# Performance work log

Hardware: AMD Instinct MI355X
Metric: run time of the kernel (lower is better)

Reference implementation:

```python
import jax, jax.numpy as jnp
import numpy as np

NE = 200000   # num_entities
NR = 16       # num_relations
D  = 128      # embed_dim
B  = 4096     # batch
S  = 64       # neighbors per node
L  = 2        # num_layers
H  = 4        # attention heads (hardcoded in module)


def _ln(x, g, b, eps=1e-5):
    m = jnp.mean(x, -1, keepdims=True)
    v = jnp.mean((x - m) ** 2, -1, keepdims=True)
    return (x - m) * jax.lax.rsqrt(v + eps) * g + b


def setup_inputs() -> dict:
    key = jax.random.key(0)
    ks = jax.random.split(key, 12)
    s = 0.05
    return {
        'drug_entity_indices': jax.random.randint(ks[0], (B,), 0, NE),
        'adj_entity': jax.random.randint(ks[1], (B, S), 0, NE),
        'adj_relation': jax.random.randint(ks[2], (B, S), 0, NR),
        'edge_weights': jax.random.uniform(ks[3], (B, S), dtype=jnp.float32),
        'entity_emb': jax.random.normal(ks[4], (NE, D), jnp.float32) * s,
        'W_rgcn': jax.random.normal(ks[5], (L, NR, D, D), jnp.float32) * s,
        'res_w': jax.random.normal(ks[6], (L, D, D), jnp.float32) * s,
        'res_b': jnp.zeros((L, D), jnp.float32),
        'proj_w': jax.random.normal(ks[7], (L, D, D), jnp.float32) * s,
        'proj_b': jnp.zeros((L, D), jnp.float32),
        'ln_g': jnp.ones((L, D), jnp.float32),
        'ln_b': jnp.zeros((L, D), jnp.float32),
        'in_proj_w': jax.random.normal(ks[8], (3 * D, D), jnp.float32) * s,
        'in_proj_b': jnp.zeros((3 * D,), jnp.float32),
        'out_proj_w': jax.random.normal(ks[9], (D, D), jnp.float32) * s,
        'out_proj_b': jnp.zeros((D,), jnp.float32),
        'fln_g': jnp.ones((D,), jnp.float32),
        'fln_b': jnp.zeros((D,), jnp.float32),
    }


def reference(drug_entity_indices, adj_entity, adj_relation, edge_weights,
              entity_emb, W_rgcn, res_w, res_b, proj_w, proj_b, ln_g, ln_b,
              in_proj_w, in_proj_b, out_proj_w, out_proj_b, fln_g, fln_b):
    node = entity_emb[drug_entity_indices]           # [B,D] combined_emb
    nbr = entity_emb[adj_entity]                     # [B,S,D]
    # Route each edge to its relation: sum_s nbr*ew*[rel==r] then one GEMM per relation
    # (mathematically identical to the per-relation masked matmul loop in torch).
    onehot = jax.nn.one_hot(adj_relation, NR, dtype=node.dtype)      # [B,S,R]
    pre = jnp.einsum('bsd,bsr->brd', nbr * edge_weights[..., None], onehot)
    outs = []
    for l in range(L):
        msgs = jnp.einsum('brd,rde->be', pre, W_rgcn[l])             # [B,D]
        h = jax.nn.relu(node + msgs + node @ res_w[l].T + res_b[l])  # RGCNAggregator
        node = _ln(h @ proj_w[l].T + proj_b[l] + node, ln_g[l], ln_b[l])
        outs.append(node)
    x = jnp.stack(outs, 0)                           # [L,B,D] seq-first
    qkv = x @ in_proj_w.T + in_proj_b
    q, k, v = jnp.split(qkv, 3, axis=-1)
    hd = D // H
    def heads(t):
        return t.reshape(L, B, H, hd).transpose(1, 2, 0, 3)          # [B,H,L,hd]
    q, k, v = heads(q), heads(k), heads(v)
    att = jax.nn.softmax(jnp.einsum('bhld,bhmd->bhlm', q, k) / np.sqrt(hd).astype(np.float32), axis=-1)
    o = jnp.einsum('bhlm,bhmd->bhld', att, v).transpose(2, 0, 1, 3).reshape(L, B, D)
    o = o @ out_proj_w.T + out_proj_b
    return _ln(o.mean(0), fln_g, fln_b)              # [B,D]
```

## Files before the change

kernel.cpp:

```cpp
#include <hip/hip_runtime.h>
#include <math.h>

#define NRREL 16
#define DDIM 128
#define BBATCH 4096
#define SNBR 64
#define ROWS 8

typedef __attribute__((ext_vector_type(8))) short short8;
typedef __attribute__((ext_vector_type(4))) float floatx4;

__device__ __forceinline__ unsigned short f2bf(float f) {
    unsigned u = __builtin_bit_cast(unsigned, f);
    u += 0x7fffu + ((u >> 16) & 1u);
    return (unsigned short)(u >> 16);
}
__device__ __forceinline__ float bf2f(unsigned short u) {
    return __builtin_bit_cast(float, ((unsigned)u) << 16);
}

extern "C" __global__ __launch_bounds__(256)
void k_prep(const float* __restrict__ W_rgcn,
            const float* __restrict__ res_w, const float* __restrict__ proj_w,
            const float* __restrict__ in_w, const float* __restrict__ out_w,
            unsigned short* __restrict__ Wcat, unsigned short* __restrict__ resw,
            unsigned short* __restrict__ projw, unsigned short* __restrict__ inw,
            unsigned short* __restrict__ outw)
{
    __shared__ float tileT[64 * 65];
    const int bid = blockIdx.x, t = threadIdx.x;

    if (bid < 128) {
        const int l = bid >> 6, rem = bid & 63;
        const int k0 = (rem >> 1) * 64, e0 = (rem & 1) * 64;
        #pragma unroll
        for (int i = 0; i < 4; ++i) {
            int flat = t + 256 * i;
            int k = flat >> 4, c = flat & 15;
            float4 v = *(const float4*)(W_rgcn + ((size_t)(l * 2048 + k0 + k)) * 128 + e0 + 4 * c);
            tileT[(4 * c + 0) * 65 + k] = v.x;
            tileT[(4 * c + 1) * 65 + k] = v.y;
            tileT[(4 * c + 2) * 65 + k] = v.z;
            tileT[(4 * c + 3) * 65 + k] = v.w;
        }
        __syncthreads();
        const int e = t >> 2, m = t & 3;
        #pragma unroll
        for (int half = 0; half < 2; ++half) {
            int kk = 16 * m + 8 * half;
            short8 o;
            #pragma unroll
            for (int j = 0; j < 8; ++j) o[j] = (short)f2bf(tileT[e * 65 + kk + j]);
            *(short8*)(Wcat + ((size_t)(l * 128 + e0 + e)) * 2048 + k0 + kk) = o;
        }
    } else {
        int j4 = ((bid - 128) * 256 + t) * 4;
        const float* src; unsigned short* dst; int off;
        if (j4 < 32768)       { src = res_w;  dst = resw;  off = j4; }
        else if (j4 < 65536)  { src = proj_w; dst = projw; off = j4 - 32768; }
        else if (j4 < 114688) { src = in_w;   dst = inw;   off = j4 - 65536; }
        else                  { src = out_w;  dst = outw;  off = j4 - 114688; }
        float4 v = *(const float4*)(src + off);
        ushort4 o = { f2bf(v.x), f2bf(v.y), f2bf(v.z), f2bf(v.w) };
        *(ushort4*)(dst + off) = o;
    }
}

extern "C" __global__ __launch_bounds__(512)
void k_fused(const int* __restrict__ drug, const int* __restrict__ adj_e,
             const int* __restrict__ adj_r, const float* __restrict__ ew,
             const float* __restrict__ emb,
             const unsigned short* __restrict__ Wcat,
             const unsigned short* __restrict__ resw, const unsigned short* __restrict__ projw,
             const float* __restrict__ res_b, const float* __restrict__ proj_b,
             const float* __restrict__ ln_g, const float* __restrict__ ln_b,
             const unsigned short* __restrict__ inw, const float* __restrict__ in_b,
             const unsigned short* __restrict__ outw, const float* __restrict__ out_b,
             const float* __restrict__ fg, const float* __restrict__ fb,
             float* __restrict__ outp)
{
    __shared__ union {
        struct { unsigned short preA[ROWS * 2056]; } a;
        struct {
            unsigned short h_b16[ROWS * 136];
            unsigned short xs_l[2 * ROWS * 136];
            unsigned short qkvl[2 * ROWS * 392];
        } t;
    } sm;
    __shared__ float node_ln[ROWS * 132];
    __shared__ unsigned short node_b16[ROWS * 136];
    __shared__ union {
        struct {
            int   cnt[ROWS][16];
            int   strt[ROWS][16];
            int   sperm[ROWS][64];
            float wperm[ROWS][64];
        } g;
        float msum[ROWS * 260];
    } sg;
    __shared__ float psum[8][8], psq[8][8];

    const int t = threadIdx.x, w = t >> 6, lane = t & 63, l15 = lane & 15, q = lane >> 4;
    const int r0 = blockIdx.x * ROWS;

    const int erow = t >> 6, es = t & 63;
    int   ent0 = adj_e[(r0 + erow) * SNBR + es];
    float ewt0 = ew[(r0 + erow) * SNBR + es];
    int   rel0 = adj_r[(r0 + erow) * SNBR + es];
    if (t < 128) sg.g.cnt[t >> 4][t & 15] = 0;
    if (t < 256) {
        int rr = t >> 5, c = t & 31;
        int di = drug[r0 + rr];
        float4 v = *(const float4*)(emb + (size_t)di * DDIM + 4 * c);
        *(float4*)(node_ln + rr * 132 + 4 * c) = v;
        ushort4 o = { f2bf(v.x), f2bf(v.y), f2bf(v.z), f2bf(v.w) };
        *(ushort4*)(node_b16 + rr * 136 + 4 * c) = o;
    }
    __syncthreads();

    atomicAdd(&sg.g.cnt[erow][rel0], 1);
    __syncthreads();

    if (t < ROWS) {
        int a = 0;
        #pragma unroll
        for (int r = 0; r < NRREL; ++r) { sg.g.strt[t][r] = a; a += sg.g.cnt[t][r]; }
    }
    __syncthreads();

    {
        int pos0 = atomicAdd(&sg.g.strt[erow][rel0], 1);
        sg.g.sperm[erow][pos0] = ent0;
        sg.g.wperm[erow][pos0] = ewt0;
    }
    __syncthreads();

    {
        #pragma unroll 1
        for (int i = 0; i < 4; ++i) {
            int u = t + 512 * i;
            int row = u >> 8, rl = (u >> 4) & 15, g8 = u & 15;
            int n = sg.g.cnt[row][rl];
            int end = sg.g.strt[row][rl];
            int beg = end - n;
            float acc[8] = {0.f, 0.f, 0.f, 0.f, 0.f, 0.f, 0.f, 0.f};
            #pragma unroll 1
            for (int jb = beg; jb < end; jb += 8) {
                const float* pp[8]; float wq[8];
                #pragma unroll
                for (int u2 = 0; u2 < 8; ++u2) {
                    int live = (jb + u2 < end);
                    int j = live ? jb + u2 : beg;
                    wq[u2] = live ? sg.g.wperm[row][j] : 0.f;
                    pp[u2] = emb + (size_t)sg.g.sperm[row][j] * DDIM + 8 * g8;
                }
                float4 v0[8], v1[8];
                #pragma unroll
                for (int u2 = 0; u2 < 8; ++u2) {
                    v0[u2] = *(const float4*)pp[u2];
                    v1[u2] = *(const float4*)(pp[u2] + 4);
                }
                #pragma unroll
                for (int u2 = 0; u2 < 8; ++u2) {
                    acc[0] = fmaf(v0[u2].x, wq[u2], acc[0]); acc[1] = fmaf(v0[u2].y, wq[u2], acc[1]);
                    acc[2] = fmaf(v0[u2].z, wq[u2], acc[2]); acc[3] = fmaf(v0[u2].w, wq[u2], acc[3]);
                    acc[4] = fmaf(v1[u2].x, wq[u2], acc[4]); acc[5] = fmaf(v1[u2].y, wq[u2], acc[5]);
                    acc[6] = fmaf(v1[u2].z, wq[u2], acc[6]); acc[7] = fmaf(v1[u2].w, wq[u2], acc[7]);
                }
            }
            short8 o;
            #pragma unroll
            for (int jj = 0; jj < 8; ++jj) o[jj] = (short)f2bf(acc[jj]);
            *(short8*)(sm.a.preA + row * 2056 + rl * DDIM + 8 * g8) = o;
        }
    }
    __syncthreads();

    {
        floatx4 macc[2] = {};
        const unsigned short* ap = sm.a.preA + (l15 & 7) * 2056 + 8 * q;
        const unsigned short* bp = Wcat + (size_t)(32 * w + l15) * 2048 + 8 * q;
        #pragma unroll 8
        for (int k = 0; k < 2048; k += 32) {
            short8 A = *(const short8*)(ap + k);
            #pragma unroll
            for (int ni = 0; ni < 2; ++ni) {
                short8 B = *(const short8*)(bp + (size_t)(ni * 16) * 2048 + k);
                macc[ni] = __builtin_amdgcn_mfma_f32_16x16x32_bf16(A, B, macc[ni], 0, 0, 0);
            }
        }
        if (q < 2) {
            #pragma unroll
            for (int ni = 0; ni < 2; ++ni) {
                int gc = 32 * w + ni * 16 + l15;
                #pragma unroll
                for (int r = 0; r < 4; ++r)
                    sg.msum[(4 * q + r) * 260 + gc] = macc[ni][r];
            }
        }
    }
    __syncthreads();

    for (int l = 0; l < 2; ++l) {
        {
            const unsigned short* Bw = resw + (size_t)l * DDIM * DDIM;
            floatx4 acc = {};
            const unsigned short* ap = node_b16 + (l15 & 7) * 136 + 8 * q;
            #pragma unroll
            for (int kk = 0; kk < DDIM; kk += 32) {
                short8 A = *(const short8*)(ap + kk);
                short8 B = *(const short8*)(Bw + (size_t)(16 * w + l15) * DDIM + kk + 8 * q);
                acc = __builtin_amdgcn_mfma_f32_16x16x32_bf16(A, B, acc, 0, 0, 0);
            }
            int gc = 16 * w + l15;
            float rb = res_b[l * DDIM + gc];
            if (q < 2) {
                #pragma unroll
                for (int r = 0; r < 4; ++r) {
                    int lr = 4 * q + r;
                    float v = acc[r] + rb + node_ln[lr * 132 + gc] + sg.msum[lr * 260 + l * DDIM + gc];
                    sm.t.h_b16[lr * 136 + gc] = f2bf(v > 0.f ? v : 0.f);
                }
            }
        }
        __syncthreads();
        {
            const unsigned short* Bw = projw + (size_t)l * DDIM * DDIM;
            floatx4 acc = {};
            const unsigned short* ap = sm.t.h_b16 + (l15 & 7) * 136 + 8 * q;
            #pragma unroll
            for (int kk = 0; kk < DDIM; kk += 32) {
                short8 A = *(const short8*)(ap + kk);
                short8 B = *(const short8*)(Bw + (size_t)(16 * w + l15) * DDIM + kk + 8 * q);
                acc = __builtin_amdgcn_mfma_f32_16x16x32_bf16(A, B, acc, 0, 0, 0);
            }
            int gc = 16 * w + l15;
            float vv[4];
            float s4[4] = {0, 0, 0, 0}, sq4[4] = {0, 0, 0, 0};
            float pb = proj_b[l * DDIM + gc];
            if (q < 2) {
                #pragma unroll
                for (int r = 0; r < 4; ++r) {
                    float v = acc[r] + pb + node_ln[(4 * q + r) * 132 + gc];
                    vv[r] = v; s4[r] = v; sq4[r] = v * v;
                }
            }
            #pragma unroll
            for (int r = 0; r < 4; ++r)
                #pragma unroll
                for (int off2 = 8; off2 >= 1; off2 >>= 1) {
                    s4[r] += __shfl_xor(s4[r], off2, 64);
                    sq4[r] += __shfl_xor(sq4[r], off2, 64);
                }
            if (l15 == 0 && q < 2) {
                #pragma unroll
                for (int r = 0; r < 4; ++r) {
                    psum[w][4 * q + r] = s4[r];
                    psq[w][4 * q + r] = sq4[r];
                }
            }
            __syncthreads();
            float g2 = ln_g[l * DDIM + gc], bb = ln_b[l * DDIM + gc];
            if (q < 2) {
                #pragma unroll
                for (int r = 0; r < 4; ++r) {
                    int lr = 4 * q + r;
                    float ssum = 0.f, ssq = 0.f;
                    #pragma unroll
                    for (int ww = 0; ww < 8; ++ww) { ssum += psum[ww][lr]; ssq += psq[ww][lr]; }
                    float mean = ssum * (1.f / DDIM);
                    float var = ssq * (1.f / DDIM) - mean * mean;
                    float val = (vv[r] - mean) * rsqrtf(var + 1e-5f) * g2 + bb;
                    node_ln[lr * 132 + gc] = val;
                    unsigned short ub = f2bf(val);
                    node_b16[lr * 136 + gc] = ub;
                    sm.t.xs_l[(2 * lr + l) * 136 + gc] = ub;
                }
            }
            __syncthreads();
        }
    }

    {
        floatx4 acc[3] = {};
        const unsigned short* ap = sm.t.xs_l + l15 * 136 + 8 * q;
        #pragma unroll
        for (int kk = 0; kk < DDIM; kk += 32) {
            short8 A = *(const short8*)(ap + kk);
            #pragma unroll
            for (int ni = 0; ni < 3; ++ni) {
                short8 B = *(const short8*)(inw + (size_t)(48 * w + ni * 16 + l15) * DDIM + kk + 8 * q);
                acc[ni] = __builtin_amdgcn_mfma_f32_16x16x32_bf16(A, B, acc[ni], 0, 0, 0);
            }
        }
        #pragma unroll
        for (int ni = 0; ni < 3; ++ni) {
            int gc = 48 * w + ni * 16 + l15;
            float ib = in_b[gc];
            #pragma unroll
            for (int r = 0; r < 4; ++r)
                sm.t.qkvl[(4 * q + r) * 392 + gc] = f2bf(acc[ni][r] + ib);
        }
    }
    __syncthreads();

    if (t < 64) {
        int g4 = t >> 3, j = t & 7;
        const unsigned short* row0 = sm.t.qkvl + (2 * g4) * 392;
        const unsigned short* row1 = row0 + 392;
        float p00 = 0.f, p01 = 0.f, p10 = 0.f, p11 = 0.f;
        #pragma unroll
        for (int dd = 0; dd < 16; ++dd) {
            int d = 16 * j + dd;
            float q0 = bf2f(row0[d]), k0 = bf2f(row0[128 + d]);
            float q1 = bf2f(row1[d]), k1 = bf2f(row1[128 + d]);
            p00 = fmaf(q0, k0, p00); p01 = fmaf(q0, k1, p01);
            p10 = fmaf(q1, k0, p10); p11 = fmaf(q1, k1, p11);
        }
        p00 += __shfl_xor(p00, 1, 64); p01 += __shfl_xor(p01, 1, 64);
        p10 += __shfl_xor(p10, 1, 64); p11 += __shfl_xor(p11, 1, 64);
        const float sc = 0.17677669529663687f;
        p00 *= sc; p01 *= sc; p10 *= sc; p11 *= sc;
        float m0 = fmaxf(p00, p01), e00 = expf(p00 - m0), e01 = expf(p01 - m0);
        float i0 = 1.f / (e00 + e01);
        float m1 = fmaxf(p10, p11), e10 = expf(p10 - m1), e11 = expf(p11 - m1);
        float i1 = 1.f / (e10 + e11);
        #pragma unroll
        for (int dd = 0; dd < 16; ++dd) {
            int d = 16 * j + dd;
            float v0 = bf2f(row0[256 + d]), v1 = bf2f(row1[256 + d]);
            sm.t.xs_l[(2 * g4) * 136 + d]     = f2bf((e00 * v0 + e01 * v1) * i0);
            sm.t.xs_l[(2 * g4 + 1) * 136 + d] = f2bf((e10 * v0 + e11 * v1) * i1);
        }
    }
    __syncthreads();

    {
        floatx4 acc = {};
        const unsigned short* ap = sm.t.xs_l + l15 * 136 + 8 * q;
        #pragma unroll
        for (int kk = 0; kk < DDIM; kk += 32) {
            short8 A = *(const short8*)(ap + kk);
            short8 B = *(const short8*)(outw + (size_t)(16 * w + l15) * DDIM + kk + 8 * q);
            acc = __builtin_amdgcn_mfma_f32_16x16x32_bf16(A, B, acc, 0, 0, 0);
        }
        int gc = 16 * w + l15;
        float ob = out_b[gc];
        float av[2];
        float s2[2], sq2[2];
        #pragma unroll
        for (int rr = 0; rr < 2; ++rr) {
            float v = 0.5f * (acc[2 * rr] + acc[2 * rr + 1]) + ob;
            av[rr] = v; s2[rr] = v; sq2[rr] = v * v;
        }
        #pragma unroll
        for (int rr = 0; rr < 2; ++rr)
            #pragma unroll
            for (int off2 = 8; off2 >= 1; off2 >>= 1) {
                s2[rr] += __shfl_xor(s2[rr], off2, 64);
                sq2[rr] += __shfl_xor(sq2[rr], off2, 64);
            }
        if (l15 == 0) {
            #pragma unroll
            for (int rr = 0; rr < 2; ++rr) {
                psum[w][2 * q + rr] = s2[rr];
                psq[w][2 * q + rr] = sq2[rr];
            }
        }
        __syncthreads();
        float g2 = fg[gc], bb = fb[gc];
        #pragma unroll
        for (int rr = 0; rr < 2; ++rr) {
            int idx = 2 * q + rr;
            float ssum = 0.f, ssq = 0.f;
            #pragma unroll
            for (int ww = 0; ww < 8; ++ww) { ssum += psum[ww][idx]; ssq += psq[ww][idx]; }
            float mean = ssum * (1.f / DDIM);
            float var = ssq * (1.f / DDIM) - mean * mean;
            outp[(size_t)(r0 + idx) * DDIM + gc] = (av[rr] - mean) * rsqrtf(var + 1e-5f) * g2 + bb;
        }
    }
}

extern "C" void kernel_launch(void* const* d_in, const int* in_sizes, int n_in,
                              void* d_out, int out_size, void* d_ws, size_t ws_size,
                              hipStream_t stream) {
    const int*   drug_idx = (const int*)d_in[0];
    const int*   adj_ent  = (const int*)d_in[1];
    const int*   adj_rel  = (const int*)d_in[2];
    const float* ew       = (const float*)d_in[3];
    const float* emb      = (const float*)d_in[4];
    const float* W_rgcn   = (const float*)d_in[5];
    const float* res_w    = (const float*)d_in[6];
    const float* res_b    = (const float*)d_in[7];
    const float* proj_w   = (const float*)d_in[8];
    const float* proj_b   = (const float*)d_in[9];
    const float* ln_g     = (const float*)d_in[10];
    const float* ln_b     = (const float*)d_in[11];
    const float* in_w     = (const float*)d_in[12];
    const float* in_b     = (const float*)d_in[13];
    const float* out_w    = (const float*)d_in[14];
    const float* out_b    = (const float*)d_in[15];
    const float* fg       = (const float*)d_in[16];
    const float* fb       = (const float*)d_in[17];
    float* outp = (float*)d_out;

    char* ws = (char*)d_ws;
    size_t off = 0;
    auto alloc = [&](size_t bytes) { size_t o = off; off = (off + bytes + 255) & ~(size_t)255; return o; };
    unsigned short* Wcat    = (unsigned short*)(ws + alloc((size_t)256 * 2048 * 2));
    unsigned short* resw    = (unsigned short*)(ws + alloc((size_t)2 * 128 * 128 * 2));
    unsigned short* projw   = (unsigned short*)(ws + alloc((size_t)2 * 128 * 128 * 2));
    unsigned short* inw     = (unsigned short*)(ws + alloc((size_t)384 * 128 * 2));
    unsigned short* outw    = (unsigned short*)(ws + alloc((size_t)128 * 128 * 2));

    hipLaunchKernelGGL(k_prep, dim3(256), dim3(256), 0, stream,
                       W_rgcn, res_w, proj_w, in_w, out_w,
                       Wcat, resw, projw, inw, outw);
    hipLaunchKernelGGL(k_fused, dim3(BBATCH / ROWS), dim3(512), 0, stream,
                       drug_idx, adj_ent, adj_rel, ew, emb,
                       Wcat, resw, projw, res_b, proj_b, ln_g, ln_b,
                       inw, in_b, outw, out_b, fg, fb, outp);
}
```

Measured before the change: 261.9 us.

## Process 16 batch rows per block with 1024 threads to fill MFMA tiles

Doubles the rows handled per block from 8 to 16 and the block size from 512 to 1024 threads. The 16x16 MFMA row dimension is now fully used instead of half wasted, so each Wcat weight tile streamed from global memory serves twice as many rows. The per-layer GEMMs, QKV projection, output projection and layer-norm reductions are remapped across 16 waves, with some waves idle in the smaller stages. Shared memory per block roughly doubles and the grid halves, which can lower occupancy and the number of blocks available to spread across CUs.

```diff
diff --git a/kernel.cpp b/kernel.cpp
--- a/kernel.cpp
+++ b/kernel.cpp
@@ -5,7 +5,7 @@
 #define DDIM 128
 #define BBATCH 4096
 #define SNBR 64
-#define ROWS 8
+#define ROWS 16
 
 typedef __attribute__((ext_vector_type(8))) short short8;
 typedef __attribute__((ext_vector_type(4))) float floatx4;
@@ -66,7 +66,7 @@
     }
 }
 
-extern "C" __global__ __launch_bounds__(512)
+extern "C" __global__ __launch_bounds__(1024)
 void k_fused(const int* __restrict__ drug, const int* __restrict__ adj_e,
              const int* __restrict__ adj_r, const float* __restrict__ ew,
              const float* __restrict__ emb,
@@ -98,7 +98,7 @@
         } g;
         float msum[ROWS * 260];
     } sg;
-    __shared__ float psum[8][8], psq[8][8];
+    __shared__ float psum[16][16], psq[16][16];
 
     const int t = threadIdx.x, w = t >> 6, lane = t & 63, l15 = lane & 15, q = lane >> 4;
     const int r0 = blockIdx.x * ROWS;
@@ -107,8 +107,8 @@
     int   ent0 = adj_e[(r0 + erow) * SNBR + es];
     float ewt0 = ew[(r0 + erow) * SNBR + es];
     int   rel0 = adj_r[(r0 + erow) * SNBR + es];
-    if (t < 128) sg.g.cnt[t >> 4][t & 15] = 0;
-    if (t < 256) {
+    if (t < 256) sg.g.cnt[t >> 4][t & 15] = 0;
+    if (t < 512) {
         int rr = t >> 5, c = t & 31;
         int di = drug[r0 + rr];
         float4 v = *(const float4*)(emb + (size_t)di * DDIM + 4 * c);
@@ -138,7 +138,7 @@
     {
         #pragma unroll 1
         for (int i = 0; i < 4; ++i) {
-            int u = t + 512 * i;
+            int u = t + 1024 * i;
             int row = u >> 8, rl = (u >> 4) & 15, g8 = u & 15;
             int n = sg.g.cnt[row][rl];
             int end = sg.g.strt[row][rl];
@@ -177,35 +177,27 @@
     __syncthreads();
 
     {
-        floatx4 macc[2] = {};
-        const unsigned short* ap = sm.a.preA + (l15 & 7) * 2056 + 8 * q;
-        const unsigned short* bp = Wcat + (size_t)(32 * w + l15) * 2048 + 8 * q;
+        floatx4 macc = {};
+        const unsigned short* ap = sm.a.preA + l15 * 2056 + 8 * q;
+        const unsigned short* bp = Wcat + (size_t)(16 * w + l15) * 2048 + 8 * q;
         #pragma unroll 8
         for (int k = 0; k < 2048; k += 32) {
             short8 A = *(const short8*)(ap + k);
-            #pragma unroll
-            for (int ni = 0; ni < 2; ++ni) {
-                short8 B = *(const short8*)(bp + (size_t)(ni * 16) * 2048 + k);
-                macc[ni] = __builtin_amdgcn_mfma_f32_16x16x32_bf16(A, B, macc[ni], 0, 0, 0);
-            }
-        }
-        if (q < 2) {
-            #pragma unroll
-            for (int ni = 0; ni < 2; ++ni) {
-                int gc = 32 * w + ni * 16 + l15;
-                #pragma unroll
-                for (int r = 0; r < 4; ++r)
-                    sg.msum[(4 * q + r) * 260 + gc] = macc[ni][r];
-            }
-        }
+            short8 B = *(const short8*)(bp + k);
+            macc = __builtin_amdgcn_mfma_f32_16x16x32_bf16(A, B, macc, 0, 0, 0);
+        }
+        int gc = 16 * w + l15;
+        #pragma unroll
+        for (int r = 0; r < 4; ++r)
+            sg.msum[(4 * q + r) * 260 + gc] = macc[r];
     }
     __syncthreads();
 
     for (int l = 0; l < 2; ++l) {
-        {
+        if (w < 8) {
             const unsigned short* Bw = resw + (size_t)l * DDIM * DDIM;
             floatx4 acc = {};
-            const unsigned short* ap = node_b16 + (l15 & 7) * 136 + 8 * q;
+            const unsigned short* ap = node_b16 + l15 * 136 + 8 * q;
             #pragma unroll
             for (int kk = 0; kk < DDIM; kk += 32) {
                 short8 A = *(const short8*)(ap + kk);
@@ -214,54 +206,52 @@
             }
             int gc = 16 * w + l15;
             float rb = res_b[l * DDIM + gc];
-            if (q < 2) {
-                #pragma unroll
-                for (int r = 0; r < 4; ++r) {
-                    int lr = 4 * q + r;
-                    float v = acc[r] + rb + node_ln[lr * 132 + gc] + sg.msum[lr * 260 + l * DDIM + gc];
-                    sm.t.h_b16[lr * 136 + gc] = f2bf(v > 0.f ? v : 0.f);
-                }
+            #pragma unroll
+            for (int r = 0; r < 4; ++r) {
+                int lr = 4 * q + r;
+                float v = acc[r] + rb + node_ln[lr * 132 + gc] + sg.msum[lr * 260 + l * DDIM + gc];
+                sm.t.h_b16[lr * 136 + gc] = f2bf(v > 0.f ? v : 0.f);
             }
         }
         __syncthreads();
         {
-            const unsigned short* Bw = projw + (size_t)l * DDIM * DDIM;
-            floatx4 acc = {};
-            const unsigned short* ap = sm.t.h_b16 + (l15 & 7) * 136 + 8 * q;
-            #pragma unroll
-            for (int kk = 0; kk < DDIM; kk += 32) {
-                short8 A = *(const short8*)(ap + kk);
-                short8 B = *(const short8*)(Bw + (size_t)(16 * w + l15) * DDIM + kk + 8 * q);
-                acc = __builtin_amdgcn_mfma_f32_16x16x32_bf16(A, B, acc, 0, 0, 0);
-            }
+            float vv[4];
             int gc = 16 * w + l15;
-            float vv[4];
-            float s4[4] = {0, 0, 0, 0}, sq4[4] = {0, 0, 0, 0};
-            float pb = proj_b[l * DDIM + gc];
-            if (q < 2) {
+            if (w < 8) {
+                const unsigned short* Bw = projw + (size_t)l * DDIM * DDIM;
+                floatx4 acc = {};
+                const unsigned short* ap = sm.t.h_b16 + l15 * 136 + 8 * q;
+                #pragma unroll
+                for (int kk = 0; kk < DDIM; kk += 32) {
+                    short8 A = *(const short8*)(ap + kk);
+                    short8 B = *(const short8*)(Bw + (size_t)(16 * w + l15) * DDIM + kk + 8 * q);
+                    acc = __builtin_amdgcn_mfma_f32_16x16x32_bf16(A, B, acc, 0, 0, 0);
+                }
+                float s4[4], sq4[4];
+                float pb = proj_b[l * DDIM + gc];
                 #pragma unroll
                 for (int r = 0; r < 4; ++r) {
                     float v = acc[r] + pb + node_ln[(4 * q + r) * 132 + gc];
                     vv[r] = v; s4[r] = v; sq4[r] = v * v;
                 }
-            }
-            #pragma unroll
-            for (int r = 0; r < 4; ++r)
-                #pragma unroll
-                for (int off2 = 8; off2 >= 1; off2 >>= 1) {
-                    s4[r] += __shfl_xor(s4[r], off2, 64);
-                    sq4[r] += __shfl_xor(sq4[r], off2, 64);
-                }
-            if (l15 == 0 && q < 2) {
-                #pragma unroll
-                for (int r = 0; r < 4; ++r) {
-                    psum[w][4 * q + r] = s4[r];
-                    psq[w][4 * q + r] = sq4[r];
+                #pragma unroll
+                for (int r = 0; r < 4; ++r)
+                    #pragma unroll
+                    for (int off2 = 8; off2 >= 1; off2 >>= 1) {
+                        s4[r] += __shfl_xor(s4[r], off2, 64);
+                        sq4[r] += __shfl_xor(sq4[r], off2, 64);
+                    }
+                if (l15 == 0) {
+                    #pragma unroll
+                    for (int r = 0; r < 4; ++r) {
+                        psum[w][4 * q + r] = s4[r];
+                        psq[w][4 * q + r] = sq4[r];
+                    }
                 }
             }
             __syncthreads();
-            float g2 = ln_g[l * DDIM + gc], bb = ln_b[l * DDIM + gc];
-            if (q < 2) {
+            if (w < 8) {
+                float g2 = ln_g[l * DDIM + gc], bb = ln_b[l * DDIM + gc];
                 #pragma unroll
                 for (int r = 0; r < 4; ++r) {
                     int lr = 4 * q + r;
@@ -281,30 +271,30 @@
         }
     }
 
-    {
-        floatx4 acc[3] = {};
-        const unsigned short* ap = sm.t.xs_l + l15 * 136 + 8 * q;
+    if (w < 12) {
+        floatx4 acc[4] = {};
+        const unsigned short* ap = sm.t.xs_l + (16 * (w & 1) + l15) * 136 + 8 * q;
         #pragma unroll
         for (int kk = 0; kk < DDIM; kk += 32) {
             short8 A = *(const short8*)(ap + kk);
             #pragma unroll
-            for (int ni = 0; ni < 3; ++ni) {
-                short8 B = *(const short8*)(inw + (size_t)(48 * w + ni * 16 + l15) * DDIM + kk + 8 * q);
+            for (int ni = 0; ni < 4; ++ni) {
+                short8 B = *(const short8*)(inw + (size_t)(64 * (w >> 1) + ni * 16 + l15) * DDIM + kk + 8 * q);
                 acc[ni] = __builtin_amdgcn_mfma_f32_16x16x32_bf16(A, B, acc[ni], 0, 0, 0);
             }
         }
         #pragma unroll
-        for (int ni = 0; ni < 3; ++ni) {
-            int gc = 48 * w + ni * 16 + l15;
+        for (int ni = 0; ni < 4; ++ni) {
+            int gc = 64 * (w >> 1) + ni * 16 + l15;
             float ib = in_b[gc];
             #pragma unroll
             for (int r = 0; r < 4; ++r)
-                sm.t.qkvl[(4 * q + r) * 392 + gc] = f2bf(acc[ni][r] + ib);
-        }
-    }
-    __syncthreads();
-
-    if (t < 64) {
+                sm.t.qkvl[(16 * (w & 1) + 4 * q + r) * 392 + gc] = f2bf(acc[ni][r] + ib);
+        }
+    }
+    __syncthreads();
+
+    if (t < 128) {
         int g4 = t >> 3, j = t & 7;
         const unsigned short* row0 = sm.t.qkvl + (2 * g4) * 392;
         const unsigned short* row1 = row0 + 392;
@@ -337,14 +327,14 @@
 
     {
         floatx4 acc = {};
-        const unsigned short* ap = sm.t.xs_l + l15 * 136 + 8 * q;
+        const unsigned short* ap = sm.t.xs_l + (16 * (w & 1) + l15) * 136 + 8 * q;
         #pragma unroll
         for (int kk = 0; kk < DDIM; kk += 32) {
             short8 A = *(const short8*)(ap + kk);
-            short8 B = *(const short8*)(outw + (size_t)(16 * w + l15) * DDIM + kk + 8 * q);
+            short8 B = *(const short8*)(outw + (size_t)(16 * (w >> 1) + l15) * DDIM + kk + 8 * q);
             acc = __builtin_amdgcn_mfma_f32_16x16x32_bf16(A, B, acc, 0, 0, 0);
         }
-        int gc = 16 * w + l15;
+        int gc = 16 * (w >> 1) + l15;
         float ob = out_b[gc];
         float av[2];
         float s2[2], sq2[2];
@@ -374,10 +364,14 @@
             int idx = 2 * q + rr;
             float ssum = 0.f, ssq = 0.f;
             #pragma unroll
-            for (int ww = 0; ww < 8; ++ww) { ssum += psum[ww][idx]; ssq += psq[ww][idx]; }
+            for (int ww = 0; ww < 8; ++ww) {
+                ssum += psum[2 * ww + (w & 1)][idx];
+                ssq  += psq[2 * ww + (w & 1)][idx];
+            }
             float mean = ssum * (1.f / DDIM);
             float var = ssq * (1.f / DDIM) - mean * mean;
-            outp[(size_t)(r0 + idx) * DDIM + gc] = (av[rr] - mean) * rsqrtf(var + 1e-5f) * g2 + bb;
+            outp[(size_t)(r0 + 8 * (w & 1) + idx) * DDIM + gc] =
+                (av[rr] - mean) * rsqrtf(var + 1e-5f) * g2 + bb;
         }
     }
 }
@@ -417,7 +411,7 @@
     hipLaunchKernelGGL(k_prep, dim3(256), dim3(256), 0, stream,
                        W_rgcn, res_w, proj_w, in_w, out_w,
                        Wcat, resw, projw, inw, outw);
-    hipLaunchKernelGGL(k_fused, dim3(BBATCH / ROWS), dim3(512), 0, stream,
+    hipLaunchKernelGGL(k_fused, dim3(BBATCH / ROWS), dim3(1024), 0, stream,
                        drug_idx, adj_ent, adj_rel, ew, emb,
                        Wcat, resw, projw, res_b, proj_b, ln_g, ln_b,
                        inw, in_b, outw, out_b, fg, fb, outp);
```

Result: faster. 232.9 us (-11.1%).
